# Kernel optimization log

Measured on AMD Instinct MI355X. Metric: run time of the kernel, lower is better.

The kernel has to match this reference:

```python
import jax, jax.numpy as jnp
import numpy as np

DIM = 768
HEADS = 12
HEAD_DIM = DIM // HEADS
SCALE = HEAD_DIM ** (-0.5)


def setup_inputs() -> dict:
    key = jax.random.key(0)
    k1, k2, k3 = jax.random.split(key, 3)
    x = jax.random.normal(k1, (4, 2048, DIM), dtype=jnp.float32)
    # nn.Linear(dim, 3*dim, bias=False): weight [3*dim, dim]
    w_qkv = jax.random.normal(k2, (3 * DIM, DIM), dtype=jnp.float32) * (DIM ** -0.5)
    # nn.Linear(dim, dim) with bias
    w_proj = jax.random.normal(k3, (DIM, DIM), dtype=jnp.float32) * (DIM ** -0.5)
    b_proj = jnp.zeros((DIM,), dtype=jnp.float32)
    return {"x": x, "w_qkv": w_qkv, "w_proj": w_proj, "b_proj": b_proj}


def reference(x, w_qkv, w_proj, b_proj):
    B, N, C = x.shape
    H, D = HEADS, HEAD_DIM
    qkv = jnp.einsum('bnc,oc->bno', x, w_qkv)  # [B,N,3C]
    qkv = qkv.reshape(B, N, 3, H, D).transpose(2, 0, 3, 1, 4)  # [3,B,H,N,D]
    q, k, v = qkv[0], qkv[1], qkv[2]
    attn = jnp.einsum('bhnd,bhmd->bhnm', q, k) * SCALE  # [B,H,N,N]
    attn = jax.nn.softmax(attn, axis=-1)
    attn = jax.nn.softmax(attn, axis=-1)  # double softmax, as in original
    out = jnp.einsum('bhnm,bhmd->bhnd', attn, v)  # [B,H,N,D]
    out = out.transpose(0, 2, 1, 3).reshape(B, N, C)
    return jnp.einsum('bnc,oc->bno', out, w_proj) + b_proj
```

## Files before the change

### kernel.cpp

```cpp
#include <hip/hip_runtime.h>
#include <hip/hip_bf16.h>

#define DIM 768
#define HEADS 12
#define HD 64
#define SEQ 2048
#define BATCH 4
#define BHN 48
#define TOK 8192

#if __has_builtin(__builtin_amdgcn_exp2f)
#define EXP2F __builtin_amdgcn_exp2f
#else
#define EXP2F exp2f
#endif
#define EXP_C 0.1803368801111244f

using short8  = __attribute__((ext_vector_type(8))) short;
using short4v = __attribute__((ext_vector_type(4))) short;
using float4v = __attribute__((ext_vector_type(4))) float;

__device__ __forceinline__ short f2b(float f) {
    union { float f; unsigned u; } v; v.f = f;
    unsigned r = v.u + 0x7FFF + ((v.u >> 16) & 1);
    return (short)(r >> 16);
}
__device__ __forceinline__ float b2f(short s) {
    union { unsigned u; float f; } v;
    v.u = ((unsigned)(unsigned short)s) << 16;
    return v.f;
}
__device__ __forceinline__ unsigned pk2(float a, float b) {
    union { float f; unsigned u; } x, y; x.f = a; y.f = b;
    return __builtin_amdgcn_perm(x.u + 0x8000u, y.u + 0x8000u, 0x03020706u);
}

typedef const __attribute__((address_space(1))) unsigned GU;
typedef __attribute__((address_space(3))) unsigned LU;
__device__ __forceinline__ void gload_lds16(const short* g, short* l) {
    __builtin_amdgcn_global_load_lds((GU*)g, (LU*)l, 16, 0, 0);
}

__global__ void cast_all(const float* __restrict__ x, const float* __restrict__ wq,
                         const float* __restrict__ wp,
                         short* __restrict__ xb, short* __restrict__ wqb,
                         short* __restrict__ wpb, int nx4, int nq4) {
    int i = blockIdx.x * 256 + threadIdx.x;
    const float* in; short* out; int j = i;
    if (i < nx4)            { in = x;  out = xb;  }
    else if (i < nx4 + nq4) { in = wq; out = wqb; j = i - nx4; }
    else                    { in = wp; out = wpb; j = i - nx4 - nq4; }
    float4 f = ((const float4*)in)[j];
    short4 o;
    o.x = f2b(f.x); o.y = f2b(f.y); o.z = f2b(f.z); o.w = f2b(f.w);
    ((short4*)out)[j] = o;
}

__global__ void vsum_kernel(const short* __restrict__ Vw, float* __restrict__ Vsum) {
    int wid  = blockIdx.x * 4 + (threadIdx.x >> 6);
    int lane = threadIdx.x & 63;
    int bh = wid >> 6, d = wid & 63;
    const short* base = Vw + (size_t)bh * (SEQ * 64) + d * 64;
    float s = 0.f;
    for (int i = lane; i < SEQ; i += 64)
        s += b2f(base[(i >> 6) * 4096 + (i & 63)]);
    #pragma unroll
    for (int m = 1; m < 64; m <<= 1) s += __shfl_xor(s, m, 64);
    if (lane == 0) Vsum[wid] = s;
}

__global__ __launch_bounds__(256, 4)
void gemm_qkv(const short* __restrict__ A, const short* __restrict__ Bw,
              short* __restrict__ Qw, short* __restrict__ Kw, short* __restrict__ Vw)
{
    __shared__ __align__(16) short As[2][128 * 32];
    __shared__ __align__(16) short Bs[2][128 * 32];

    const int tid  = threadIdx.x;
    const int lane = tid & 63;
    const int wave = tid >> 6;
    const int wm = (wave >> 1) * 64, wn = (wave & 1) * 64;
    const int l15 = lane & 15, quad = lane >> 4;

    const int gid = blockIdx.x;
    const int w   = gid >> 3;
    const int ybl = (gid & 7) * 8 + (w & 7);
    const int xbl = w >> 3;

    const bool vpart = (xbl >= 12);
    const short* rowsP = vpart ? (Bw + 1536 * 768) : A;
    const short* colsP = vpart ? A : Bw;
    const int m0 = vpart ? (xbl - 12) * 128 : ybl * 128;
    const int n0 = vpart ? ybl * 128 : xbl * 128;
    const int K = DIM;

    float4v acc[4][4];
    #pragma unroll
    for (int i = 0; i < 4; i++)
        #pragma unroll
        for (int j = 0; j < 4; j++)
            acc[i][j] = (float4v){0.f, 0.f, 0.f, 0.f};

    const int G0 = wave * 128 + lane;
    const int G1 = G0 + 64;
    const int rA0 = G0 >> 2, cA0 = (G0 & 3) * 8;
    const int rA1 = G1 >> 2, cA1 = (G1 & 3) * 8;
    const int ldsoff = wave * 1024;

    for (int kt = 0; kt < K; kt += 64) {
        #pragma unroll
        for (int s = 0; s < 2; s++) {
            const int kc = kt + s * 32;
            gload_lds16(&rowsP[(size_t)(m0 + rA0) * K + kc + cA0], &As[s][ldsoff]);
            gload_lds16(&rowsP[(size_t)(m0 + rA1) * K + kc + cA1], &As[s][ldsoff + 512]);
            gload_lds16(&colsP[(size_t)(n0 + rA0) * K + kc + cA0], &Bs[s][ldsoff]);
            gload_lds16(&colsP[(size_t)(n0 + rA1) * K + kc + cA1], &Bs[s][ldsoff + 512]);
        }
        __syncthreads();
        #pragma unroll
        for (int s = 0; s < 2; s++) {
            short8 af[4], bfr[4];
            #pragma unroll
            for (int t = 0; t < 4; t++) {
                af[t]  = *(const short8*)&As[s][(wm + t * 16 + l15) * 32 + quad * 8];
                bfr[t] = *(const short8*)&Bs[s][(wn + t * 16 + l15) * 32 + quad * 8];
            }
            #pragma unroll
            for (int tm = 0; tm < 4; tm++)
                #pragma unroll
                for (int tn = 0; tn < 4; tn++)
                    acc[tm][tn] = __builtin_amdgcn_mfma_f32_16x16x32_bf16(af[tm], bfr[tn], acc[tm][tn], 0, 0, 0);
        }
        __syncthreads();
    }

    #pragma unroll
    for (int tm = 0; tm < 4; tm++)
        #pragma unroll
        for (int tn = 0; tn < 4; tn++)
            #pragma unroll
            for (int r = 0; r < 4; r++) {
                int row = m0 + wm + tm * 16 + quad * 4 + r;
                int col = n0 + wn + tn * 16 + l15;
                float v = acc[tm][tn][r];
                if (vpart) {
                    int hh = row >> 6, d = row & 63;
                    int b = col >> 11, n = col & 2047;
                    int bh = b * HEADS + hh;
                    int t2 = n >> 6, c2h = (n >> 5) & 1, wk = n & 31;
                    int slot = ((wk & 15) >> 2) * 8 + ((wk & 16) >> 2) + (wk & 3);
                    int g2 = c2h * 4 + (slot >> 3);
                    int gp2 = g2 ^ (d & 7);
                    Vw[(size_t)bh * (SEQ * 64) + t2 * 4096 + d * 64 + gp2 * 8 + (slot & 7)] = f2b(v);
                } else {
                    int hh = (col & 767) >> 6, d = col & 63;
                    int b = row >> 11, n = row & 2047;
                    int bh = b * HEADS + hh;
                    size_t idx = (size_t)bh * (SEQ * 64) + (size_t)n * 64
                               + (((d >> 3) ^ (n & 7)) << 3) + (d & 7);
                    if (col < 768) Qw[idx] = f2b(v * EXP_C);
                    else           Kw[idx] = f2b(v);
                }
            }
}

__global__ __launch_bounds__(256, 4)
void gemm_proj(const short* __restrict__ A, const short* __restrict__ Bw,
               const float* __restrict__ bias, float* __restrict__ Out)
{
    __shared__ __align__(16) short As[2][128 * 32];
    __shared__ __align__(16) short Bs[2][64 * 32];

    const int tid  = threadIdx.x;
    const int lane = tid & 63;
    const int wave = tid >> 6;
    const int wm = (wave >> 1) * 64, wn = (wave & 1) * 32;
    const int l15 = lane & 15, quad = lane >> 4;

    const int gid = blockIdx.x;
    const int w   = gid >> 3;
    const int ybl = (gid & 7) * 8 + (w & 7);
    const int xbl = w >> 3;
    const int m0 = ybl * 128, n0 = xbl * 64;
    const int K = DIM;

    float4v acc[4][2];
    #pragma unroll
    for (int i = 0; i < 4; i++)
        #pragma unroll
        for (int j = 0; j < 2; j++)
            acc[i][j] = (float4v){0.f, 0.f, 0.f, 0.f};

    const int GA0 = wave * 128 + lane, GA1 = GA0 + 64;
    const int rA0 = GA0 >> 2, cA0 = (GA0 & 3) * 8;
    const int rA1 = GA1 >> 2, cA1 = (GA1 & 3) * 8;
    const int GB0 = wave * 64 + lane;
    const int rB0 = GB0 >> 2, cB0 = (GB0 & 3) * 8;
    const int ldsoffA = wave * 1024, ldsoffB = wave * 512;

    for (int kt = 0; kt < K; kt += 64) {
        #pragma unroll
        for (int s = 0; s < 2; s++) {
            const int kc = kt + s * 32;
            gload_lds16(&A [(size_t)(m0 + rA0) * K + kc + cA0], &As[s][ldsoffA]);
            gload_lds16(&A [(size_t)(m0 + rA1) * K + kc + cA1], &As[s][ldsoffA + 512]);
            gload_lds16(&Bw[(size_t)(n0 + rB0) * K + kc + cB0], &Bs[s][ldsoffB]);
        }
        __syncthreads();
        #pragma unroll
        for (int s = 0; s < 2; s++) {
            short8 af[4], bfr[2];
            #pragma unroll
            for (int t = 0; t < 4; t++)
                af[t] = *(const short8*)&As[s][(wm + t * 16 + l15) * 32 + quad * 8];
            #pragma unroll
            for (int t = 0; t < 2; t++)
                bfr[t] = *(const short8*)&Bs[s][(wn + t * 16 + l15) * 32 + quad * 8];
            #pragma unroll
            for (int tm = 0; tm < 4; tm++)
                #pragma unroll
                for (int tn = 0; tn < 2; tn++)
                    acc[tm][tn] = __builtin_amdgcn_mfma_f32_16x16x32_bf16(af[tm], bfr[tn], acc[tm][tn], 0, 0, 0);
        }
        __syncthreads();
    }

    #pragma unroll
    for (int tm = 0; tm < 4; tm++)
        #pragma unroll
        for (int tn = 0; tn < 2; tn++)
            #pragma unroll
            for (int r = 0; r < 4; r++) {
                int row = m0 + wm + tm * 16 + quad * 4 + r;
                int col = n0 + wn + tn * 16 + l15;
                Out[(size_t)row * 768 + col] = acc[tm][tn][r] + bias[col];
            }
}

__global__ __launch_bounds__(256, 4)
void attn_kernel(const short* __restrict__ Qw, const short* __restrict__ Kw,
                 const short* __restrict__ Vw, const float* __restrict__ Vsum,
                 short* __restrict__ Ow)
{
    __shared__ __align__(16) short LDS[16384];

    const int tid  = threadIdx.x;
    const int lane = tid & 63, wave = tid >> 6;
    const int l15 = lane & 15, quad = lane >> 4;
    const int r7  = l15 & 7;
    const int bid = blockIdx.x;
    const int ii  = bid >> 3;
    const int bh  = (bid & 7) * 6 + (ii >> 4);
    const int qt  = ii & 15;
    const int wq  = wave * 32;

    const short* Qp = Qw + (size_t)bh * (SEQ * 64) + qt * 8192;
    const short* Kp = Kw + (size_t)bh * (SEQ * 64);
    const short* Vp = Vw + (size_t)bh * (SEQ * 64);

    short8 onesf;
    #pragma unroll
    for (int j = 0; j < 8; j++) onesf[j] = (l15 == 0) ? (short)0x3F80 : (short)0;

    #pragma unroll
    for (int h = 0; h < 4; h++) {
        const int g = wave * 4 + h;
        gload_lds16(&Qp[g * 512 + lane * 8], &LDS[g * 512]);
    }
    __syncthreads();
    short8 aq[2][2];
    #pragma unroll
    for (int nb = 0; nb < 2; nb++)
        #pragma unroll
        for (int kk = 0; kk < 2; kk++) {
            int r = wq + nb * 16 + l15;
            aq[nb][kk] = *(const short8*)&LDS[r * 64 + (((kk * 4 + quad) ^ r7) << 3)];
        }
    __syncthreads();

    float4v Aacc[2][4], Lacc[2];
    #pragma unroll
    for (int mb = 0; mb < 2; mb++) {
        Lacc[mb] = (float4v){0.f, 0.f, 0.f, 0.f};
        #pragma unroll
        for (int t = 0; t < 4; t++) Aacc[mb][t] = (float4v){0.f, 0.f, 0.f, 0.f};
    }

    auto STAGE = [&](int t2, int kbuf) {
        const int kb = kbuf * 4096;
        #pragma unroll
        for (int h = 0; h < 2; h++) {
            const int g = wave * 2 + h;
            gload_lds16(&Kp[(size_t)t2 * 4096 + g * 512 + lane * 8], &LDS[kb + g * 512]);
            gload_lds16(&Vp[(size_t)t2 * 4096 + g * 512 + lane * 8], &LDS[8192 + kb + g * 512]);
        }
    };

    STAGE(0, 0);
    STAGE(1, 1);

    for (int kt = 0; kt < 32; kt++) {
        if (kt < 31) { asm volatile("s_waitcnt vmcnt(4)" ::: "memory"); }
        else         { asm volatile("s_waitcnt vmcnt(0)" ::: "memory"); }
        __builtin_amdgcn_sched_barrier(0);
        __builtin_amdgcn_s_barrier();
        __builtin_amdgcn_sched_barrier(0);

        const int kb = (kt & 1) * 4096;
        const short* KB = &LDS[kb];
        const short* VB = &LDS[8192 + kb];

        #pragma unroll
        for (int c2 = 0; c2 < 2; c2++) {
            union AE { unsigned u[4]; short8 s; };
            AE ae[2];
            #pragma unroll
            for (int tn2 = 0; tn2 < 2; tn2++) {
                const int row = (c2 * 2 + tn2) * 16 + l15;
                const short* rp = &KB[row * 64];
                short8 b0 = *(const short8*)&rp[(quad ^ r7) << 3];
                short8 b1 = *(const short8*)&rp[((4 + quad) ^ r7) << 3];
                #pragma unroll
                for (int nb = 0; nb < 2; nb++) {
                    float4v s = (float4v){0.f, 0.f, 0.f, 0.f};
                    s = __builtin_amdgcn_mfma_f32_16x16x32_bf16(b0, aq[nb][0], s, 0, 0, 0);
                    s = __builtin_amdgcn_mfma_f32_16x16x32_bf16(b1, aq[nb][1], s, 0, 0, 0);
                    ae[nb].u[tn2 * 2]     = pk2(EXP2F(s[0]), EXP2F(s[1]));
                    ae[nb].u[tn2 * 2 + 1] = pk2(EXP2F(s[2]), EXP2F(s[3]));
                }
            }
            __builtin_amdgcn_s_setprio(1);
            Lacc[0] = __builtin_amdgcn_mfma_f32_16x16x32_bf16(ae[0].s, onesf, Lacc[0], 0, 0, 0);
            Lacc[1] = __builtin_amdgcn_mfma_f32_16x16x32_bf16(ae[1].s, onesf, Lacc[1], 0, 0, 0);
            #pragma unroll
            for (int tn = 0; tn < 4; tn++) {
                const int d = tn * 16 + l15;
                short8 bv = *(const short8*)&VB[d * 64 + (((c2 * 4 + quad) ^ r7) << 3)];
                Aacc[0][tn] = __builtin_amdgcn_mfma_f32_16x16x32_bf16(ae[0].s, bv, Aacc[0][tn], 0, 0, 0);
                Aacc[1][tn] = __builtin_amdgcn_mfma_f32_16x16x32_bf16(ae[1].s, bv, Aacc[1][tn], 0, 0, 0);
            }
            __builtin_amdgcn_s_setprio(0);
        }

        __builtin_amdgcn_sched_barrier(0);
        __builtin_amdgcn_s_barrier();
        __builtin_amdgcn_sched_barrier(0);
        if (kt < 30) STAGE(kt + 2, kt & 1);
    }

    const int b = bh / HEADS, hh = bh - (bh / HEADS) * HEADS;
    #pragma unroll
    for (int mb = 0; mb < 2; mb++)
        #pragma unroll
        for (int r = 0; r < 4; r++) {
            float il = 1.f / __shfl(Lacc[mb][r], lane & 48, 64);
            int row = qt * 128 + wq + mb * 16 + quad * 4 + r;
            int tok = b * SEQ + row;
            #pragma unroll
            for (int tn = 0; tn < 4; tn++) {
                int d = tn * 16 + l15;
                float vs = Vsum[bh * 64 + d];
                float val = (vs + Aacc[mb][tn][r] * il) * (1.f / 2049.f);
                Ow[(size_t)tok * 768 + hh * 64 + d] = f2b(val);
            }
        }
}

extern "C" void kernel_launch(void* const* d_in, const int* in_sizes, int n_in,
                              void* d_out, int out_size, void* d_ws, size_t ws_size,
                              hipStream_t stream) {
    const float* x      = (const float*)d_in[0];
    const float* w_qkv  = (const float*)d_in[1];
    const float* w_proj = (const float*)d_in[2];
    const float* b_proj = (const float*)d_in[3];
    float* out = (float*)d_out;

    char* ws = (char*)d_ws;
    size_t off = 0;
    auto alloc = [&](size_t bytes) {
        void* p = ws + off;
        off += (bytes + 255) & ~(size_t)255;
        return p;
    };
    short* x_bf  = (short*)alloc((size_t)TOK * DIM * 2);
    short* wq_bf = (short*)alloc((size_t)3 * DIM * DIM * 2);
    short* wp_bf = (short*)alloc((size_t)DIM * DIM * 2);
    short* Qw    = (short*)alloc((size_t)BHN * SEQ * 64 * 2);
    short* Kw    = (short*)alloc((size_t)BHN * SEQ * 64 * 2);
    short* Vw    = (short*)alloc((size_t)BHN * SEQ * 64 * 2);
    short* Ow    = (short*)alloc((size_t)TOK * DIM * 2);
    float* Vsum  = (float*)alloc((size_t)BHN * 64 * 4);

    int nx4 = TOK * DIM / 4, nq4 = 3 * DIM * DIM / 4, np4 = DIM * DIM / 4;
    int tot4 = nx4 + nq4 + np4;
    cast_all<<<tot4 / 256, 256, 0, stream>>>(x, w_qkv, w_proj, x_bf, wq_bf, wp_bf, nx4, nq4);

    gemm_qkv<<<1152, 256, 0, stream>>>(x_bf, wq_bf, Qw, Kw, Vw);

    vsum_kernel<<<BHN * 64 / 4, 256, 0, stream>>>(Vw, Vsum);

    attn_kernel<<<BHN * 16, 256, 0, stream>>>(Qw, Kw, Vw, Vsum, Ow);

    gemm_proj<<<768, 256, 0, stream>>>(Ow, wp_bf, b_proj, out);
}
```

Baseline: 206.0 us.

## Fuse V column sums into QKV GEMM, triple-buffer attention K/V tiles

Removes the separate vsum kernel by reducing V accumulators in the QKV GEMM epilogue and adding them with float atomics; Vsum is zeroed inside the cast kernel. The attention kernel moves from double to triple LDS buffering, which drops the end-of-iteration barrier, and lowers the occupancy hint to 3 blocks. The row-sum MFMA against a ones vector is replaced by scalar accumulation of the exp values plus a shuffle reduction. In exchange this adds atomic contention, gives non-deterministic summation order, and lowers occupancy.

```diff
diff --git a/kernel.cpp b/kernel.cpp
--- a/kernel.cpp
+++ b/kernel.cpp
@@ -44,8 +44,10 @@
 __global__ void cast_all(const float* __restrict__ x, const float* __restrict__ wq,
                          const float* __restrict__ wp,
                          short* __restrict__ xb, short* __restrict__ wqb,
-                         short* __restrict__ wpb, int nx4, int nq4) {
+                         short* __restrict__ wpb, float* __restrict__ Vsum,
+                         int nx4, int nq4) {
     int i = blockIdx.x * 256 + threadIdx.x;
+    if (i < BHN * 64) Vsum[i] = 0.f;
     const float* in; short* out; int j = i;
     if (i < nx4)            { in = x;  out = xb;  }
     else if (i < nx4 + nq4) { in = wq; out = wqb; j = i - nx4; }
@@ -56,22 +58,10 @@
     ((short4*)out)[j] = o;
 }
 
-__global__ void vsum_kernel(const short* __restrict__ Vw, float* __restrict__ Vsum) {
-    int wid  = blockIdx.x * 4 + (threadIdx.x >> 6);
-    int lane = threadIdx.x & 63;
-    int bh = wid >> 6, d = wid & 63;
-    const short* base = Vw + (size_t)bh * (SEQ * 64) + d * 64;
-    float s = 0.f;
-    for (int i = lane; i < SEQ; i += 64)
-        s += b2f(base[(i >> 6) * 4096 + (i & 63)]);
-    #pragma unroll
-    for (int m = 1; m < 64; m <<= 1) s += __shfl_xor(s, m, 64);
-    if (lane == 0) Vsum[wid] = s;
-}
-
 __global__ __launch_bounds__(256, 4)
 void gemm_qkv(const short* __restrict__ A, const short* __restrict__ Bw,
-              short* __restrict__ Qw, short* __restrict__ Kw, short* __restrict__ Vw)
+              short* __restrict__ Qw, short* __restrict__ Kw, short* __restrict__ Vw,
+              float* __restrict__ Vsum)
 {
     __shared__ __align__(16) short As[2][128 * 32];
     __shared__ __align__(16) short Bs[2][128 * 32];
@@ -162,6 +152,23 @@
                     else           Kw[idx] = f2b(v);
                 }
             }
+
+    if (vpart) {
+        const int bb = n0 >> 11;
+        #pragma unroll
+        for (int tm = 0; tm < 4; tm++)
+            #pragma unroll
+            for (int r = 0; r < 4; r++) {
+                float s4 = (acc[tm][0][r] + acc[tm][1][r]) + (acc[tm][2][r] + acc[tm][3][r]);
+                #pragma unroll
+                for (int m = 1; m < 16; m <<= 1) s4 += __shfl_xor(s4, m, 64);
+                if (l15 == 0) {
+                    int row = m0 + wm + tm * 16 + quad * 4 + r;
+                    int hh = row >> 6, d = row & 63;
+                    atomicAdd(&Vsum[(bb * HEADS + hh) * 64 + d], s4);
+                }
+            }
+    }
 }
 
 __global__ __launch_bounds__(256, 4)
@@ -237,12 +244,12 @@
             }
 }
 
-__global__ __launch_bounds__(256, 4)
+__global__ __launch_bounds__(256, 3)
 void attn_kernel(const short* __restrict__ Qw, const short* __restrict__ Kw,
                  const short* __restrict__ Vw, const float* __restrict__ Vsum,
                  short* __restrict__ Ow)
 {
-    __shared__ __align__(16) short LDS[16384];
+    __shared__ __align__(16) short LDS[24576];
 
     const int tid  = threadIdx.x;
     const int lane = tid & 63, wave = tid >> 6;
@@ -258,10 +265,6 @@
     const short* Kp = Kw + (size_t)bh * (SEQ * 64);
     const short* Vp = Vw + (size_t)bh * (SEQ * 64);
 
-    short8 onesf;
-    #pragma unroll
-    for (int j = 0; j < 8; j++) onesf[j] = (l15 == 0) ? (short)0x3F80 : (short)0;
-
     #pragma unroll
     for (int h = 0; h < 4; h++) {
         const int g = wave * 4 + h;
@@ -278,13 +281,12 @@
         }
     __syncthreads();
 
-    float4v Aacc[2][4], Lacc[2];
-    #pragma unroll
-    for (int mb = 0; mb < 2; mb++) {
-        Lacc[mb] = (float4v){0.f, 0.f, 0.f, 0.f};
+    float4v Aacc[2][4];
+    float Lp[2] = {0.f, 0.f};
+    #pragma unroll
+    for (int mb = 0; mb < 2; mb++)
         #pragma unroll
         for (int t = 0; t < 4; t++) Aacc[mb][t] = (float4v){0.f, 0.f, 0.f, 0.f};
-    }
 
     auto STAGE = [&](int t2, int kbuf) {
         const int kb = kbuf * 4096;
@@ -292,13 +294,14 @@
         for (int h = 0; h < 2; h++) {
             const int g = wave * 2 + h;
             gload_lds16(&Kp[(size_t)t2 * 4096 + g * 512 + lane * 8], &LDS[kb + g * 512]);
-            gload_lds16(&Vp[(size_t)t2 * 4096 + g * 512 + lane * 8], &LDS[8192 + kb + g * 512]);
+            gload_lds16(&Vp[(size_t)t2 * 4096 + g * 512 + lane * 8], &LDS[12288 + kb + g * 512]);
         }
     };
 
     STAGE(0, 0);
     STAGE(1, 1);
 
+    int cur = 0, nx2 = 2;
     for (int kt = 0; kt < 32; kt++) {
         if (kt < 31) { asm volatile("s_waitcnt vmcnt(4)" ::: "memory"); }
         else         { asm volatile("s_waitcnt vmcnt(0)" ::: "memory"); }
@@ -306,9 +309,8 @@
         __builtin_amdgcn_s_barrier();
         __builtin_amdgcn_sched_barrier(0);
 
-        const int kb = (kt & 1) * 4096;
-        const short* KB = &LDS[kb];
-        const short* VB = &LDS[8192 + kb];
+        const short* KB = &LDS[cur * 4096];
+        const short* VB = &LDS[12288 + cur * 4096];
 
         #pragma unroll
         for (int c2 = 0; c2 < 2; c2++) {
@@ -325,13 +327,14 @@
                     float4v s = (float4v){0.f, 0.f, 0.f, 0.f};
                     s = __builtin_amdgcn_mfma_f32_16x16x32_bf16(b0, aq[nb][0], s, 0, 0, 0);
                     s = __builtin_amdgcn_mfma_f32_16x16x32_bf16(b1, aq[nb][1], s, 0, 0, 0);
-                    ae[nb].u[tn2 * 2]     = pk2(EXP2F(s[0]), EXP2F(s[1]));
-                    ae[nb].u[tn2 * 2 + 1] = pk2(EXP2F(s[2]), EXP2F(s[3]));
+                    float e0 = EXP2F(s[0]), e1 = EXP2F(s[1]);
+                    float e2 = EXP2F(s[2]), e3 = EXP2F(s[3]);
+                    Lp[nb] += (e0 + e1) + (e2 + e3);
+                    ae[nb].u[tn2 * 2]     = pk2(e0, e1);
+                    ae[nb].u[tn2 * 2 + 1] = pk2(e2, e3);
                 }
             }
             __builtin_amdgcn_s_setprio(1);
-            Lacc[0] = __builtin_amdgcn_mfma_f32_16x16x32_bf16(ae[0].s, onesf, Lacc[0], 0, 0, 0);
-            Lacc[1] = __builtin_amdgcn_mfma_f32_16x16x32_bf16(ae[1].s, onesf, Lacc[1], 0, 0, 0);
             #pragma unroll
             for (int tn = 0; tn < 4; tn++) {
                 const int d = tn * 16 + l15;
@@ -342,10 +345,16 @@
             __builtin_amdgcn_s_setprio(0);
         }
 
-        __builtin_amdgcn_sched_barrier(0);
-        __builtin_amdgcn_s_barrier();
-        __builtin_amdgcn_sched_barrier(0);
-        if (kt < 30) STAGE(kt + 2, kt & 1);
+        if (kt < 30) STAGE(kt + 2, nx2);
+        cur = (cur == 2) ? 0 : cur + 1;
+        nx2 = (nx2 == 2) ? 0 : nx2 + 1;
+    }
+
+    float Lfull[2];
+    #pragma unroll
+    for (int nb = 0; nb < 2; nb++) {
+        float t = Lp[nb] + __shfl_xor(Lp[nb], 16, 64);
+        Lfull[nb] = t + __shfl_xor(t, 32, 64);
     }
 
     const int b = bh / HEADS, hh = bh - (bh / HEADS) * HEADS;
@@ -353,7 +362,7 @@
     for (int mb = 0; mb < 2; mb++)
         #pragma unroll
         for (int r = 0; r < 4; r++) {
-            float il = 1.f / __shfl(Lacc[mb][r], lane & 48, 64);
+            float il = 1.f / __shfl(Lfull[mb], quad * 4 + r, 64);
             int row = qt * 128 + wq + mb * 16 + quad * 4 + r;
             int tok = b * SEQ + row;
             #pragma unroll
@@ -393,11 +402,9 @@
 
     int nx4 = TOK * DIM / 4, nq4 = 3 * DIM * DIM / 4, np4 = DIM * DIM / 4;
     int tot4 = nx4 + nq4 + np4;
-    cast_all<<<tot4 / 256, 256, 0, stream>>>(x, w_qkv, w_proj, x_bf, wq_bf, wp_bf, nx4, nq4);
-
-    gemm_qkv<<<1152, 256, 0, stream>>>(x_bf, wq_bf, Qw, Kw, Vw);
-
-    vsum_kernel<<<BHN * 64 / 4, 256, 0, stream>>>(Vw, Vsum);
+    cast_all<<<tot4 / 256, 256, 0, stream>>>(x, w_qkv, w_proj, x_bf, wq_bf, wp_bf, Vsum, nx4, nq4);
+
+    gemm_qkv<<<1152, 256, 0, stream>>>(x_bf, wq_bf, Qw, Kw, Vw, Vsum);
 
     attn_kernel<<<BHN * 16, 256, 0, stream>>>(Qw, Kw, Vw, Vsum, Ow);
 
```

After: 204.1 us. Within noise of the previous version (-0.9%).
